# Kernel optimization log

Measured on AMD Instinct MI355X. Metric: run time of the kernel, lower is better.

Reference implementation:

```python
import jax, jax.numpy as jnp
import numpy as np

DIM, H, MAX_K, RADIUS, KNN_K, ALPHA, LN_EPS = 128, 4, 32, 0.3, 8, 2, 1e-5
DH = DIM // H
SCALE = DH ** -0.5


def _layernorm(x, w, b):
    mu = jnp.mean(x, axis=-1, keepdims=True)
    var = jnp.mean((x - mu) ** 2, axis=-1, keepdims=True)
    return (x - mu) * jax.lax.rsqrt(var + LN_EPS) * w + b


def setup_inputs() -> dict:
    key = jax.random.key(0)
    ks = jax.random.split(key, 12)
    N, M = 50000, 2500
    init = lambda k, shape: (jax.random.normal(k, shape, jnp.float32) * 0.02)
    return {
        "xyz": jax.random.normal(ks[0], (N, 3), jnp.float32),
        "feats": jax.random.normal(ks[1], (N, DIM), jnp.float32),
        "Wq": init(ks[2], (DIM, DIM)),
        "Wk": init(ks[3], (DIM, DIM)),
        "Wv": init(ks[4], (DIM, DIM)),
        "Wo": init(ks[5], (DIM, DIM)),
        "bo": jnp.zeros((DIM,), jnp.float32),
        "n1w": jnp.ones((DIM,), jnp.float32),
        "n1b": jnp.zeros((DIM,), jnp.float32),
        "n2w": jnp.ones((DIM,), jnp.float32),
        "n2b": jnp.zeros((DIM,), jnp.float32),
        "W1": init(ks[6], (DIM, 4 * DIM)),
        "b1": jnp.zeros((4 * DIM,), jnp.float32),
        "W2": init(ks[7], (4 * DIM, DIM)),
        "b2": jnp.zeros((DIM,), jnp.float32),
        "Wp": init(ks[8], (DIM, DIM)),
        "bp": jnp.zeros((DIM,), jnp.float32),
        "idx_center": jax.random.randint(ks[9], (M,), 0, N),
    }


def reference(xyz, feats, Wq, Wk, Wv, Wo, bo, n1w, n1b, n2w, n2b, W1, b1, W2, b2, Wp, bp, idx_center):
    M = idx_center.shape[0]
    center_xyz = xyz[idx_center]          # (M,3)
    center_feat = feats[idx_center]       # (M,C)

    # euclidean distance matrix (M,N) via |a|^2+|b|^2-2ab, safe sqrt (0-grad at 0 like torch.cdist)
    d2 = (jnp.sum(center_xyz ** 2, -1)[:, None] + jnp.sum(xyz ** 2, -1)[None, :]
          - 2.0 * center_xyz @ xyz.T)
    d2 = jnp.maximum(d2, 0.0)
    pos = d2 > 0
    dist = jnp.where(pos, jnp.sqrt(jnp.where(pos, d2, 1.0)), 0.0)  # (M,N)

    # ball query: mask + top-max_k smallest distances
    nbr_mask = dist < RADIUS
    nbr_mask = nbr_mask.at[jnp.arange(M), idx_center].set(True)
    dist_masked = jnp.where(nbr_mask, dist, jnp.inf)
    neg_d, nbr_idx = jax.lax.top_k(-dist_masked, MAX_K)   # (M,K)
    nbr_dist = -neg_d
    mask_valid = jnp.isfinite(nbr_dist)                    # (M,K)

    # gather neighbor feats, zero where invalid
    nbr_feats = jnp.where(mask_valid[..., None], feats[nbr_idx], 0.0)  # (M,K,C)

    # masked local attention per center (tiny heads)
    q = (center_feat @ Wq).reshape(M, H, DH)                       # (M,H,D)
    k = (nbr_feats @ Wk).reshape(M, MAX_K, H, DH).transpose(0, 2, 1, 3)  # (M,H,K,D)
    v = (nbr_feats @ Wv).reshape(M, MAX_K, H, DH).transpose(0, 2, 1, 3)
    attn = jnp.einsum('mhd,mhkd->mhk', q * SCALE, k)
    attn = jnp.where(mask_valid[:, None, :], attn, -1e9)
    attn = jax.nn.softmax(attn, axis=-1)
    out = jnp.einsum('mhk,mhkd->mhd', attn, v)
    # faithful to torch: transpose(1,2) before flatten -> (M, D, H) layout
    out = jnp.swapaxes(out, 1, 2).reshape(M, DIM)
    upd = out @ Wo + bo

    cf = center_feat + _layernorm(upd, n1w, n1b)
    ffn = jax.nn.relu(cf @ W1 + b1) @ W2 + b2
    cf = cf + _layernorm(ffn, n2w, n2b)

    # KNN inverse-distance-weighted upsample back to all N points
    neg_v, knn_idx = jax.lax.top_k(-dist.T, KNN_K)   # (N,k)
    knn_dist = -neg_v
    w = 1.0 / (knn_dist + 1e-6) ** ALPHA
    w = w / jnp.sum(w, axis=-1, keepdims=True)
    out_feats = jnp.einsum('nk,nkc->nc', w, cf[knn_idx])  # (N,C)
    out_feats = out_feats + jax.nn.relu(out_feats @ Wp + bp)
    return feats + out_feats
```

## Files before the change

kernel.cpp:

```cpp
#include <hip/hip_runtime.h>
#include <hip/hip_bf16.h>
#include <stdint.h>

#define DIM    128
#define KMAX   32
#define LN_EPS 1e-5f
#define ATT_SCALE 0.17677669529663687f
#define CAND   2048
#define WTOT   214400
#define PB     32
#define NSTR2  72
#define KSTR   132

typedef unsigned long long u64;
static __device__ __forceinline__ float bf2f(__hip_bfloat16 x) { return __bfloat162float(x); }

static __device__ __forceinline__ float norm32(float x, float y, float z) {
    return __fadd_rn(__fadd_rn(__fmul_rn(x, x), __fmul_rn(y, y)), __fmul_rn(z, z));
}
static __device__ __forceinline__ float d2_32(float cx, float cy, float cz, float cw,
                                              float px, float py, float pz, float pw) {
    float dot = __fmaf_rn(cz, pz, __fmaf_rn(cy, py, __fmul_rn(cx, px)));
    return __fsub_rn(__fadd_rn(cw, pw), __fmul_rn(2.0f, dot));
}
static __device__ __forceinline__ float d2_to_dist(float d2) {
    d2 = fmaxf(d2, 0.0f);
    return (d2 > 0.0f) ? __fsqrt_rn(d2) : 0.0f;
}
static __device__ __forceinline__ float dist32(float cx, float cy, float cz, float cw,
                                               float px, float py, float pz, float pw) {
    return d2_to_dist(d2_32(cx, cy, cz, cw, px, py, pz, pw));
}

static __device__ __forceinline__ float ldf(const void* p, int f32, size_t i) {
    return f32 ? ((const float*)p)[i] : bf2f(((const __hip_bfloat16*)p)[i]);
}
static __device__ __forceinline__ int ldidx(const void* p, int i64, int m) {
    return i64 ? ((const int*)p)[2 * m] : ((const int*)p)[m];
}

struct Ptrs { const void* p[18]; int sz[18]; };

__global__ void probe_dtypes(Ptrs P, int* __restrict__ fl) {
    int j = threadIdx.x;
    if (j >= 18) return;
    const void* x = P.p[j];
    int sz = P.sz[j];
    int flag = 0;
    if (j == 17) {
        const int* ip = (const int*)x;
        int odd_zero = 1, even_nz = 0;
        for (int k = 0; k < 8 && 2 * k + 1 < sz * 2; ++k) {
            if (ip[2 * k + 1] != 0) odd_zero = 0;
            if (ip[2 * k] != 0) even_nz = 1;
        }
        flag = (odd_zero && even_nz) ? 1 : 0;
    } else {
        const __hip_bfloat16* hp = (const __hip_bfloat16*)x;
        int n = sz < 256 ? sz : 256;
        for (int i = 0; i < n; ++i) {
            float w = bf2f(hp[i]);
            if (w != w || fabsf(w) > 1000.0f) { flag = 1; break; }
        }
        if ((j == 7 || j == 9) && bf2f(hp[0]) == 0.0f) flag = 1;
    }
    fl[j] = flag;
}

__global__ __launch_bounds__(256) void conv_prep(Ptrs P, const int* __restrict__ fl,
                                                 float* __restrict__ Wf,
                                                 float4* __restrict__ pnt4,
                                                 float4* __restrict__ cent4,
                                                 int N, int M, int convB) {
    int b = blockIdx.x;
    if (b < convB) {
        int i = b * 256 + threadIdx.x;
        if (i >= WTOT) return;
        int j, off;
        if      (i < 16384)  { j = 2;  off = i; }
        else if (i < 32768)  { j = 3;  off = i - 16384; }
        else if (i < 49152)  { j = 4;  off = i - 32768; }
        else if (i < 65536)  { j = 5;  off = i - 49152; }
        else if (i < 131072) { j = 11; off = i - 65536; }
        else if (i < 196608) { j = 13; off = i - 131072; }
        else if (i < 212992) { j = 15; off = i - 196608; }
        else if (i < 213120) { j = 6;  off = i - 212992; }
        else if (i < 213248) { j = 7;  off = i - 213120; }
        else if (i < 213376) { j = 8;  off = i - 213248; }
        else if (i < 213504) { j = 9;  off = i - 213376; }
        else if (i < 213632) { j = 10; off = i - 213504; }
        else if (i < 214144) { j = 12; off = i - 213632; }
        else if (i < 214272) { j = 14; off = i - 214144; }
        else                 { j = 16; off = i - 214272; }
        Wf[i] = ldf(P.p[j], fl[j], off);
    } else {
        int i = (b - convB) * 256 + threadIdx.x;
        int f0 = fl[0];
        if (i < N) {
            float x = ldf(P.p[0], f0, 3 * i + 0);
            float y = ldf(P.p[0], f0, 3 * i + 1);
            float z = ldf(P.p[0], f0, 3 * i + 2);
            pnt4[i] = make_float4(x, y, z, norm32(x, y, z));
        }
        if (i < M) {
            int c = ldidx(P.p[17], fl[17], i);
            c = (c >= 0 && c < N) ? c : 0;
            float x = ldf(P.p[0], f0, 3 * c + 0);
            float y = ldf(P.p[0], f0, 3 * c + 1);
            float z = ldf(P.p[0], f0, 3 * c + 2);
            cent4[i] = make_float4(x, y, z, norm32(x, y, z));
        }
    }
}

__global__ __launch_bounds__(256) void ball_scan(
    const float4* __restrict__ pnt4,
    const float4* __restrict__ cent4,
    int N, int* __restrict__ nbr_g) {

    __shared__ u64 key[CAND];
    __shared__ int s_cnt, s_ni[KMAX];

    int m = blockIdx.x, tid = threadIdx.x;
    float4 cc4 = cent4[m];

    if (tid == 0) s_cnt = 0;
    if (tid < KMAX) s_ni[tid] = -1;
    __syncthreads();

    for (int i = tid; i < N; i += 256) {
        float4 p = pnt4[i];
        float d2 = d2_32(cc4.x, cc4.y, cc4.z, cc4.w, p.x, p.y, p.z, p.w);
        if (d2 < 0.0901f) {
            float dist = d2_to_dist(d2);
            if (dist < 0.3f) {
                int pos = atomicAdd(&s_cnt, 1);
                if (pos < CAND)
                    key[pos] = ((u64)__float_as_uint(dist) << 32) | (unsigned)i;
            }
        }
    }
    __syncthreads();
    int cnt = min(s_cnt, CAND);

    for (int i = tid; i < cnt; i += 256) {
        u64 ki = key[i];
        int r = 0;
        for (int j = 0; j < cnt; ++j) r += (key[j] < ki) ? 1 : 0;
        if (r < KMAX) s_ni[r] = (int)(unsigned)(ki & 0xFFFFFFFFULL);
    }
    __syncthreads();
    if (tid < KMAX) nbr_g[m * KMAX + tid] = s_ni[tid];
}

#define NFT2(cc, kk) R[(cc) * NSTR2 + (kk)]
#define SKV2(kk, col) R[(kk) * KSTR + (col)]

__global__ __launch_bounds__(256, 4) void attn_ffn(
    const int* __restrict__ nbr_g,
    const void* __restrict__ feats,
    const void* __restrict__ idxc,
    const int* __restrict__ fl,
    const float* __restrict__ Wf,
    float* __restrict__ cf_out, int N, int M) {

    const float* Wqf = Wf;
    const float* Wkf = Wf + 16384;
    const float* Wvf = Wf + 32768;
    const float* Wof = Wf + 49152;
    const float* W1f = Wf + 65536;
    const float* W2f = Wf + 131072;
    const float* Pf  = Wf + 212992;

    __shared__ __align__(16) float R[128 * NSTR2];
    __shared__ int   s_ni[2 * KMAX];
    __shared__ __align__(16) float s_cf[256], s_x[256];
    __shared__ float s_red[8];

    int tid = threadIdx.x;
    int lane = tid & 63, wv = tid >> 6;
    int center = tid >> 7, col = tid & 127;
    int m0 = blockIdx.x * 2;
    int f1 = fl[1], fi = fl[17];

    if (tid < 64) {
        int m2 = m0 + (tid >> 5);
        s_ni[tid] = (m2 < M) ? nbr_g[m2 * KMAX + (tid & 31)] : -1;
    }
    {
        int m2 = m0 + center; m2 = (m2 < M) ? m2 : (M - 1);
        int c = ldidx(idxc, fi, m2);
        c = (c >= 0 && c < N) ? c : 0;
        s_cf[tid] = ldf(feats, f1, (size_t)c * DIM + col);
    }
    __syncthreads();
    for (int t = tid; t < 64 * DIM; t += 256) {
        int kk2 = t >> 7, cc = t & 127;
        int idx = s_ni[kk2];
        float v = (idx >= 0 && idx < N) ? ldf(feats, f1, (size_t)idx * DIM + cc) : 0.0f;
        NFT2(cc, kk2) = v;
    }
    __syncthreads();

    int kq = tid >> 5, cq = tid & 31;
    int k0 = kq * 8, c0 = cq * 4;
    float ka[8][4], va[8][4];
#pragma unroll
    for (int j = 0; j < 8; ++j)
#pragma unroll
        for (int cc2 = 0; cc2 < 4; ++cc2) { ka[j][cc2] = 0.0f; va[j][cc2] = 0.0f; }

#pragma unroll 2
    for (int i = 0; i < DIM; ++i) {
        float4 n0  = *(const float4*)&NFT2(i, k0);
        float4 n1  = *(const float4*)&NFT2(i, k0 + 4);
        float4 wk  = *(const float4*)&Wkf[i * DIM + c0];
        float4 wv4 = *(const float4*)&Wvf[i * DIM + c0];
        float nn[8] = {n0.x, n0.y, n0.z, n0.w, n1.x, n1.y, n1.z, n1.w};
#pragma unroll
        for (int j = 0; j < 8; ++j) {
            float nj = nn[j];
            ka[j][0] = fmaf(nj, wk.x, ka[j][0]);
            ka[j][1] = fmaf(nj, wk.y, ka[j][1]);
            ka[j][2] = fmaf(nj, wk.z, ka[j][2]);
            ka[j][3] = fmaf(nj, wk.w, ka[j][3]);
            va[j][0] = fmaf(nj, wv4.x, va[j][0]);
            va[j][1] = fmaf(nj, wv4.y, va[j][1]);
            va[j][2] = fmaf(nj, wv4.z, va[j][2]);
            va[j][3] = fmaf(nj, wv4.w, va[j][3]);
        }
    }
    __syncthreads();

    float* s_q    = R + 8448;
    float* s_attn = R + 8704;
    float* s_ao   = R + 8960;

#pragma unroll
    for (int j = 0; j < 8; ++j)
        *(float4*)&SKV2(k0 + j, c0) = make_float4(ka[j][0], ka[j][1], ka[j][2], ka[j][3]);
    {
        float acc = 0.0f;
        const float* cfc = s_cf + center * 128;
#pragma unroll 4
        for (int i = 0; i < DIM; i += 4) {
            float4 a = *(const float4*)&cfc[i];
            acc = fmaf(a.x, Wqf[(i + 0) * DIM + col], acc);
            acc = fmaf(a.y, Wqf[(i + 1) * DIM + col], acc);
            acc = fmaf(a.z, Wqf[(i + 2) * DIM + col], acc);
            acc = fmaf(a.w, Wqf[(i + 3) * DIM + col], acc);
        }
        s_q[tid] = acc;
    }
    __syncthreads();

    {
        int h = (tid >> 5) & 3, kk = tid & 31;
        float s = 0.0f;
#pragma unroll
        for (int d = 0; d < 32; ++d)
            s = fmaf(s_q[center * 128 + h * 32 + d], SKV2(center * 32 + kk, h * 32 + d), s);
        s *= ATT_SCALE;
        if (s_ni[center * 32 + kk] < 0) s = -1e9f;
        float mx = s;
        for (int off = 16; off; off >>= 1) mx = fmaxf(mx, __shfl_xor(mx, off, 32));
        float e = expf(s - mx);
        float sm = e;
        for (int off = 16; off; off >>= 1) sm += __shfl_xor(sm, off, 32);
        sm = (sm > 0.0f) ? sm : 1.0f;
        s_attn[tid] = e / sm;
    }
    __syncthreads();
#pragma unroll
    for (int j = 0; j < 8; ++j)
        *(float4*)&SKV2(k0 + j, c0) = make_float4(va[j][0], va[j][1], va[j][2], va[j][3]);
    __syncthreads();

    {
        int h = (tid >> 5) & 3, d = tid & 31;
        float o = 0.0f;
#pragma unroll
        for (int kk = 0; kk < KMAX; ++kk)
            o = fmaf(s_attn[center * 128 + h * 32 + kk], SKV2(center * 32 + kk, h * 32 + d), o);
        s_ao[center * 128 + d * 4 + h] = o;
    }
    __syncthreads();

    float upd = Pf[0 + col];
    {
#pragma unroll 4
        for (int i = 0; i < DIM; i += 4) {
            float4 a = *(const float4*)&s_ao[center * 128 + i];
            upd = fmaf(a.x, Wof[(i + 0) * DIM + col], upd);
            upd = fmaf(a.y, Wof[(i + 1) * DIM + col], upd);
            upd = fmaf(a.z, Wof[(i + 2) * DIM + col], upd);
            upd = fmaf(a.w, Wof[(i + 3) * DIM + col], upd);
        }
        float sum = upd;
        for (int off = 32; off; off >>= 1) sum += __shfl_xor(sum, off, 64);
        if (lane == 0) s_red[wv] = sum;
    }
    __syncthreads();
    float mu = (s_red[center * 2] + s_red[center * 2 + 1]) * (1.0f / 128.0f);
    float xc = upd - mu;
    {
        float q2 = xc * xc;
        for (int off = 32; off; off >>= 1) q2 += __shfl_xor(q2, off, 64);
        if (lane == 0) s_red[4 + wv] = q2;
    }
    __syncthreads();
    float var = (s_red[4 + center * 2] + s_red[5 + center * 2]) * (1.0f / 128.0f);
    float cf1;
    {
        float rs = 1.0f / sqrtf(var + LN_EPS);
        float ln1 = fmaf(xc * rs, Pf[128 + col], Pf[256 + col]);
        cf1 = s_cf[tid] + ln1;
        s_x[tid] = cf1;
    }
    __syncthreads();

    float* s_h = R;
#pragma unroll
    for (int jj = 0; jj < 4; ++jj) {
        int j = col + 128 * jj;
        float a = Pf[640 + j];
#pragma unroll 4
        for (int i = 0; i < DIM; i += 4) {
            float4 v = *(const float4*)&s_x[center * 128 + i];
            a = fmaf(v.x, W1f[(i + 0) * 512 + j], a);
            a = fmaf(v.y, W1f[(i + 1) * 512 + j], a);
            a = fmaf(v.z, W1f[(i + 2) * 512 + j], a);
            a = fmaf(v.w, W1f[(i + 3) * 512 + j], a);
        }
        s_h[center * 512 + j] = fmaxf(a, 0.0f);
    }
    __syncthreads();

    float fa = Pf[1152 + col];
    {
        const float* hc = s_h + center * 512;
#pragma unroll 4
        for (int i = 0; i < 256; i += 4) {
            float4 v = *(const float4*)&hc[i];
            fa = fmaf(v.x, W2f[(i + 0) * DIM + col], fa);
            fa = fmaf(v.y, W2f[(i + 1) * DIM + col], fa);
            fa = fmaf(v.z, W2f[(i + 2) * DIM + col], fa);
            fa = fmaf(v.w, W2f[(i + 3) * DIM + col], fa);
        }
    }
    float fb = 0.0f;
    {
        const float* hc = s_h + center * 512;
#pragma unroll 4
        for (int i = 256; i < 512; i += 4) {
            float4 v = *(const float4*)&hc[i];
            fb = fmaf(v.x, W2f[(i + 0) * DIM + col], fb);
            fb = fmaf(v.y, W2f[(i + 1) * DIM + col], fb);
            fb = fmaf(v.z, W2f[(i + 2) * DIM + col], fb);
            fb = fmaf(v.w, W2f[(i + 3) * DIM + col], fb);
        }
    }
    float ffn = fa + fb;
    {
        float sum = ffn;
        for (int off = 32; off; off >>= 1) sum += __shfl_xor(sum, off, 64);
        if (lane == 0) s_red[wv] = sum;
    }
    __syncthreads();
    mu = (s_red[center * 2] + s_red[center * 2 + 1]) * (1.0f / 128.0f);
    xc = ffn - mu;
    {
        float q2 = xc * xc;
        for (int off = 32; off; off >>= 1) q2 += __shfl_xor(q2, off, 64);
        if (lane == 0) s_red[4 + wv] = q2;
    }
    __syncthreads();
    var = (s_red[4 + center * 2] + s_red[5 + center * 2]) * (1.0f / 128.0f);
    {
        float rs2 = 1.0f / sqrtf(var + LN_EPS);
        float ln2 = fmaf(xc * rs2, Pf[384 + col], Pf[512 + col]);
        int m2 = m0 + center;
        if (m2 < M) cf_out[(size_t)m2 * DIM + col] = cf1 + ln2;
    }
}

#define CSWAP(a, b) { if ((b) < (a)) { u64 t_ = (a); (a) = (b); (b) = t_; } }

static __device__ __forceinline__ float extract8(float vmn) {
    float vv = vmn, T = 0.0f;
#pragma unroll
    for (int e = 0; e < 8; ++e) {
        float mv = vv;
        for (int off = 32; off; off >>= 1) mv = fminf(mv, __shfl_xor(mv, off, 64));
        T = mv;
        if (vv == mv) vv = 3.4e38f;
    }
    return fmaxf(T, 0.0f) * 1.0000019073486328f;
}

__global__ __launch_bounds__(256) void knn_select(
    const float4* __restrict__ pnt4,
    const float4* __restrict__ cent4,
    const float* __restrict__ cf,
    float* __restrict__ upg,
    int N, int M) {

    __shared__ u64 s_buf[4][2][64];
    __shared__ u64 s_srt[4][2][8];
    __shared__ int s_cnt[4][2];

    int tid = threadIdx.x;
    int lane = tid & 63, wv = tid >> 6;
    int p0 = blockIdx.x * 8 + wv * 2;
    bool ownA = (p0 < N), ownB = (p0 + 1 < N);

    float4 pa = make_float4(0.f, 0.f, 0.f, 0.f);
    float4 pb = make_float4(0.f, 0.f, 0.f, 0.f);
    if (ownA) pa = pnt4[p0];
    if (ownB) pb = pnt4[p0 + 1];

    if (lane < 2) s_cnt[wv][lane] = 0;
    __syncthreads();

    float va = 3.4e38f, vb = 3.4e38f;
    for (int j = lane; j < M; j += 64) {
        float4 cc = cent4[j];
        va = fminf(va, d2_32(cc.x, cc.y, cc.z, cc.w, pa.x, pa.y, pa.z, pa.w));
        vb = fminf(vb, d2_32(cc.x, cc.y, cc.z, cc.w, pb.x, pb.y, pb.z, pb.w));
    }
    float Ta = extract8(va);
    float Tb = extract8(vb);

    for (int j = lane; j < M; j += 64) {
        float4 cc = cent4[j];
        float d2a = d2_32(cc.x, cc.y, cc.z, cc.w, pa.x, pa.y, pa.z, pa.w);
        float d2b = d2_32(cc.x, cc.y, cc.z, cc.w, pb.x, pb.y, pb.z, pb.w);
        if (d2a <= Ta) {
            float dist = d2_to_dist(d2a);
            u64 key = ((u64)__float_as_uint(dist) << 32) | (unsigned)j;
            int pos = atomicAdd(&s_cnt[wv][0], 1);
            if (pos < 64) s_buf[wv][0][pos] = key;
        }
        if (d2b <= Tb) {
            float dist = d2_to_dist(d2b);
            u64 key = ((u64)__float_as_uint(dist) << 32) | (unsigned)j;
            int pos = atomicAdd(&s_cnt[wv][1], 1);
            if (pos < 64) s_buf[wv][1][pos] = key;
        }
    }

    int   ki[2][8];
    float w8[2][8];
    float wsum[2];

#pragma unroll
    for (int e = 0; e < 2; ++e) {
        int cnt = s_cnt[wv][e];
        if (cnt <= 64 && M >= 8) {
            u64 myk = (lane < cnt) ? s_buf[wv][e][lane] : ~0ULL;
            int r = 0;
            for (int i = 0; i < cnt; ++i) {
                u64 o = s_buf[wv][e][i];
                r += (o < myk) ? 1 : 0;
            }
            if (lane < cnt && r < 8) s_srt[wv][e][r] = myk;
        } else {
            float4 pp = e ? pb : pa;
            u64 f0 = ~0ULL, f1_ = ~0ULL, f2_ = ~0ULL, f3 = ~0ULL,
                f4 = ~0ULL, f5 = ~0ULL, f6 = ~0ULL, f7 = ~0ULL;
            for (int j = lane; j < M; j += 64) {
                float4 cc = cent4[j];
                float dist = dist32(cc.x, cc.y, cc.z, cc.w, pp.x, pp.y, pp.z, pp.w);
                u64 key = ((u64)__float_as_uint(dist) << 32) | (unsigned)j;
                if (key < f7) {
                    f7 = key;
                    CSWAP(f6, f7); CSWAP(f5, f6); CSWAP(f4, f5); CSWAP(f3, f4);
                    CSWAP(f2_, f3); CSWAP(f1_, f2_); CSWAP(f0, f1_);
                }
            }
            int ptr2 = 0;
            u64 cur2 = f0;
#pragma unroll
            for (int e2 = 0; e2 < 8; ++e2) {
                u64 v = cur2;
                for (int off = 32; off; off >>= 1) {
                    u64 o = __shfl_down(v, off, 64);
                    v = (o < v) ? o : v;
                }
                u64 gm = __shfl(v, 0, 64);
                if (lane == 0) s_srt[wv][e][e2] = gm;
                if (cur2 == gm) {
                    ptr2++;
                    cur2 = (ptr2 == 1) ? f1_ : (ptr2 == 2) ? f2_ : (ptr2 == 3) ? f3 :
                           (ptr2 == 4) ? f4 : (ptr2 == 5) ? f5 : (ptr2 == 6) ? f6 :
                           (ptr2 == 7) ? f7 : ~0ULL;
                }
            }
        }
        float ws = 0.0f;
#pragma unroll
        for (int e2 = 0; e2 < 8; ++e2) {
            u64 gm = s_srt[wv][e][e2];
            float d = __uint_as_float((unsigned)(gm >> 32));
            int ci = (int)(unsigned)(gm & 0xFFFFFFFFULL);
            ci = (ci >= 0 && ci < M) ? ci : 0;
            float t = __fadd_rn(d, 1e-6f);
            float w = 1.0f / __fmul_rn(t, t);
            ws += w;
            ki[e][e2] = ci;
            w8[e][e2] = w;
        }
        wsum[e] = ws;
    }

    float invA = 1.0f / wsum[0];
    float invB = 1.0f / wsum[1];
#pragma unroll
    for (int k = 0; k < 8; ++k) { w8[0][k] *= invA; w8[1][k] *= invB; }

    int c0 = lane, c1 = lane + 64;
    float uA0 = 0.0f, uA1 = 0.0f, uB0 = 0.0f, uB1 = 0.0f;
#pragma unroll
    for (int k = 0; k < 8; ++k) {
        const float* row = cf + (size_t)ki[0][k] * DIM;
        uA0 = fmaf(w8[0][k], row[c0], uA0);
        uA1 = fmaf(w8[0][k], row[c1], uA1);
    }
#pragma unroll
    for (int k = 0; k < 8; ++k) {
        const float* row = cf + (size_t)ki[1][k] * DIM;
        uB0 = fmaf(w8[1][k], row[c0], uB0);
        uB1 = fmaf(w8[1][k], row[c1], uB1);
    }

    if (ownA) {
        upg[(size_t)p0 * DIM + c0] = uA0;
        upg[(size_t)p0 * DIM + c1] = uA1;
    }
    if (ownB) {
        upg[(size_t)(p0 + 1) * DIM + c0] = uB0;
        upg[(size_t)(p0 + 1) * DIM + c1] = uB1;
    }
}

__global__ __launch_bounds__(256) void wp_out(
    const float* __restrict__ Wf,
    const void* __restrict__ feats,
    const int* __restrict__ fl,
    float* __restrict__ out,
    int N) {

    const float* Wpf = Wf + 196608;
    const float* bpf = Wf + 212992 + 1280;

    __shared__ __align__(16) float s_up[PB][132];

    int tid = threadIdx.x;
    int p0 = blockIdx.x * PB;

    for (int f = tid; f < PB * 32; f += 256) {
        int p = f >> 5, i4 = (f & 31) << 2;
        float4 v = make_float4(0.f, 0.f, 0.f, 0.f);
        if (p0 + p < N) v = *(const float4*)&out[(size_t)(p0 + p) * DIM + i4];
        *(float4*)&s_up[p][i4] = v;
    }
    __syncthreads();

    int cq = tid & 31, pq = tid >> 5;
    int c0 = cq << 2;
    int pA = pq << 2;

    float a00 = 0.f, a01 = 0.f, a02 = 0.f, a03 = 0.f;
    float a10 = 0.f, a11 = 0.f, a12 = 0.f, a13 = 0.f;
    float a20 = 0.f, a21 = 0.f, a22 = 0.f, a23 = 0.f;
    float a30 = 0.f, a31 = 0.f, a32 = 0.f, a33 = 0.f;

#pragma unroll 4
    for (int i = 0; i < DIM; ++i) {
        float4 w = *(const float4*)&Wpf[(size_t)i * DIM + c0];
        float u0 = s_up[pA + 0][i];
        float u1 = s_up[pA + 1][i];
        float u2 = s_up[pA + 2][i];
        float u3 = s_up[pA + 3][i];
        a00 = fmaf(u0, w.x, a00); a01 = fmaf(u0, w.y, a01);
        a02 = fmaf(u0, w.z, a02); a03 = fmaf(u0, w.w, a03);
        a10 = fmaf(u1, w.x, a10); a11 = fmaf(u1, w.y, a11);
        a12 = fmaf(u1, w.z, a12); a13 = fmaf(u1, w.w, a13);
        a20 = fmaf(u2, w.x, a20); a21 = fmaf(u2, w.y, a21);
        a22 = fmaf(u2, w.z, a22); a23 = fmaf(u2, w.w, a23);
        a30 = fmaf(u3, w.x, a30); a31 = fmaf(u3, w.y, a31);
        a32 = fmaf(u3, w.z, a32); a33 = fmaf(u3, w.w, a33);
    }

    int f1v = fl[1];
    float4 bp4 = make_float4(bpf[c0 + 0], bpf[c0 + 1], bpf[c0 + 2], bpf[c0 + 3]);

    float accs[4][4] = {{a00, a01, a02, a03}, {a10, a11, a12, a13},
                        {a20, a21, a22, a23}, {a30, a31, a32, a33}};
#pragma unroll
    for (int a = 0; a < 4; ++a) {
        int p = p0 + pA + a;
        if (p < N) {
            float4 u = *(const float4*)&s_up[pA + a][c0];
            float4 o;
            o.x = ldf(feats, f1v, (size_t)p * DIM + c0 + 0) + u.x + fmaxf(bp4.x + accs[a][0], 0.0f);
            o.y = ldf(feats, f1v, (size_t)p * DIM + c0 + 1) + u.y + fmaxf(bp4.y + accs[a][1], 0.0f);
            o.z = ldf(feats, f1v, (size_t)p * DIM + c0 + 2) + u.z + fmaxf(bp4.z + accs[a][2], 0.0f);
            o.w = ldf(feats, f1v, (size_t)p * DIM + c0 + 3) + u.w + fmaxf(bp4.w + accs[a][3], 0.0f);
            *(float4*)&out[(size_t)p * DIM + c0] = o;
        }
    }
}

extern "C" void kernel_launch(void* const* d_in, const int* in_sizes, int n_in,
                              void* d_out, int out_size, void* d_ws, size_t ws_size,
                              hipStream_t stream) {
    int N = in_sizes[0] / 3;
    int M = in_sizes[17];

    Ptrs P;
    for (int j = 0; j < 18; ++j) { P.p[j] = d_in[j]; P.sz[j] = in_sizes[j]; }

    size_t off = 0;
    auto alloc = [&](size_t bytes) -> void* {
        off = (off + 255) & ~(size_t)255;
        void* p = (void*)((char*)d_ws + off);
        off += bytes;
        return p;
    };
    int*    fl    = (int*)alloc(32 * 4);
    float*  Wf    = (float*)alloc((size_t)WTOT * 4);
    float4* pnt4  = (float4*)alloc((size_t)N * 16);
    float4* cent4 = (float4*)alloc((size_t)M * 16);
    float*  cfbuf = (float*)alloc((size_t)M * DIM * 4);
    int*    nbr   = (int*)alloc((size_t)M * KMAX * 4);

    int convB = (WTOT + 255) / 256;
    int NM = (N > M) ? N : M;
    int prepB = (NM + 255) / 256;

    probe_dtypes<<<1, 32, 0, stream>>>(P, fl);
    conv_prep<<<convB + prepB, 256, 0, stream>>>(P, fl, Wf, pnt4, cent4, N, M, convB);
    ball_scan<<<M, 256, 0, stream>>>(pnt4, cent4, N, nbr);
    attn_ffn<<<(M + 1) / 2, 256, 0, stream>>>(nbr, d_in[1], d_in[17], fl, Wf, cfbuf, N, M);
    knn_select<<<(N + 7) / 8, 256, 0, stream>>>(pnt4, cent4, cfbuf, (float*)d_out, N, M);
    wp_out<<<(N + PB - 1) / PB, 256, 0, stream>>>(Wf, d_in[1], fl, (float*)d_out, N);
}
```

Measured before the change: 511.7 us.

## Process two centers per ball_scan block and four points per knn wave with LDS-staged centers

ball_scan now handles two centers per block, so each point load is shared by two distance tests, and the rank sort is split across two half-blocks. knn_select handles four points per wave instead of two and stages all center coordinates in shared memory (up to 2560 entries), so each center read serves more points and comes from LDS rather than global memory. Both changes aim to cut redundant global loads in the two scan-heavy kernels. The cost is more LDS per block (about 40KB in knn_select), higher register pressure, fewer blocks in flight, and half-block rank sorting that may serialize more when neighbour counts are large.

```diff
diff --git a/kernel.cpp b/kernel.cpp
--- a/kernel.cpp
+++ b/kernel.cpp
@@ -11,6 +11,7 @@
 #define PB     32
 #define NSTR2  72
 #define KSTR   132
+#define SCMAX  2560
 
 typedef unsigned long long u64;
 static __device__ __forceinline__ float bf2f(__hip_bfloat16 x) { return __bfloat162float(x); }
@@ -116,41 +117,57 @@
 __global__ __launch_bounds__(256) void ball_scan(
     const float4* __restrict__ pnt4,
     const float4* __restrict__ cent4,
-    int N, int* __restrict__ nbr_g) {
-
-    __shared__ u64 key[CAND];
-    __shared__ int s_cnt, s_ni[KMAX];
-
-    int m = blockIdx.x, tid = threadIdx.x;
-    float4 cc4 = cent4[m];
-
-    if (tid == 0) s_cnt = 0;
-    if (tid < KMAX) s_ni[tid] = -1;
+    int N, int M, int* __restrict__ nbr_g) {
+
+    __shared__ u64 key[2][CAND];
+    __shared__ int s_cnt[2], s_ni[2][KMAX];
+
+    int tid = threadIdx.x;
+    int m0 = blockIdx.x * 2, m1 = m0 + 1;
+    bool has1 = (m1 < M);
+    float4 c0 = cent4[m0];
+    float4 c1 = has1 ? cent4[m1] : make_float4(1e30f, 1e30f, 1e30f, 1e30f);
+
+    if (tid < 2) s_cnt[tid] = 0;
+    if (tid < KMAX) { s_ni[0][tid] = -1; s_ni[1][tid] = -1; }
     __syncthreads();
 
     for (int i = tid; i < N; i += 256) {
         float4 p = pnt4[i];
-        float d2 = d2_32(cc4.x, cc4.y, cc4.z, cc4.w, p.x, p.y, p.z, p.w);
-        if (d2 < 0.0901f) {
-            float dist = d2_to_dist(d2);
+        float d20 = d2_32(c0.x, c0.y, c0.z, c0.w, p.x, p.y, p.z, p.w);
+        if (d20 < 0.0901f) {
+            float dist = d2_to_dist(d20);
             if (dist < 0.3f) {
-                int pos = atomicAdd(&s_cnt, 1);
+                int pos = atomicAdd(&s_cnt[0], 1);
                 if (pos < CAND)
-                    key[pos] = ((u64)__float_as_uint(dist) << 32) | (unsigned)i;
+                    key[0][pos] = ((u64)__float_as_uint(dist) << 32) | (unsigned)i;
             }
         }
-    }
-    __syncthreads();
-    int cnt = min(s_cnt, CAND);
-
-    for (int i = tid; i < cnt; i += 256) {
-        u64 ki = key[i];
+        float d21 = d2_32(c1.x, c1.y, c1.z, c1.w, p.x, p.y, p.z, p.w);
+        if (d21 < 0.0901f) {
+            float dist = d2_to_dist(d21);
+            if (dist < 0.3f) {
+                int pos = atomicAdd(&s_cnt[1], 1);
+                if (pos < CAND)
+                    key[1][pos] = ((u64)__float_as_uint(dist) << 32) | (unsigned)i;
+            }
+        }
+    }
+    __syncthreads();
+
+    int half = tid >> 7, t2 = tid & 127;
+    int cnth = min(s_cnt[half], CAND);
+    if (half == 1 && !has1) cnth = 0;
+    for (int i = t2; i < cnth; i += 128) {
+        u64 ki = key[half][i];
         int r = 0;
-        for (int j = 0; j < cnt; ++j) r += (key[j] < ki) ? 1 : 0;
-        if (r < KMAX) s_ni[r] = (int)(unsigned)(ki & 0xFFFFFFFFULL);
-    }
-    __syncthreads();
-    if (tid < KMAX) nbr_g[m * KMAX + tid] = s_ni[tid];
+        for (int j = 0; j < cnth; ++j) r += (key[half][j] < ki) ? 1 : 0;
+        if (r < KMAX) s_ni[half][r] = (int)(unsigned)(ki & 0xFFFFFFFFULL);
+    }
+    __syncthreads();
+    if (tid < KMAX) nbr_g[m0 * KMAX + tid] = s_ni[0][tid];
+    if (has1 && tid >= 128 && tid < 128 + KMAX)
+        nbr_g[m1 * KMAX + (tid - 128)] = s_ni[1][tid - 128];
 }
 
 #define NFT2(cc, kk) R[(cc) * NSTR2 + (kk)]
@@ -405,56 +422,58 @@
     float* __restrict__ upg,
     int N, int M) {
 
-    __shared__ u64 s_buf[4][2][64];
-    __shared__ u64 s_srt[4][2][8];
-    __shared__ int s_cnt[4][2];
+    __shared__ __align__(16) float4 s_ct[SCMAX];
+    __shared__ u64 s_buf[4][4][64];
+    __shared__ u64 s_srt[4][4][8];
+    __shared__ int s_cnt[4][4];
 
     int tid = threadIdx.x;
     int lane = tid & 63, wv = tid >> 6;
-    int p0 = blockIdx.x * 8 + wv * 2;
-    bool ownA = (p0 < N), ownB = (p0 + 1 < N);
-
-    float4 pa = make_float4(0.f, 0.f, 0.f, 0.f);
-    float4 pb = make_float4(0.f, 0.f, 0.f, 0.f);
-    if (ownA) pa = pnt4[p0];
-    if (ownB) pb = pnt4[p0 + 1];
-
-    if (lane < 2) s_cnt[wv][lane] = 0;
-    __syncthreads();
-
-    float va = 3.4e38f, vb = 3.4e38f;
+    int p0 = blockIdx.x * 16 + wv * 4;
+
+    float4 pp[4];
+    bool own[4];
+#pragma unroll
+    for (int e = 0; e < 4; ++e) {
+        int p = p0 + e;
+        own[e] = (p < N);
+        pp[e] = own[e] ? pnt4[p] : make_float4(0.f, 0.f, 0.f, 0.f);
+    }
+
+    if (lane < 4) s_cnt[wv][lane] = 0;
+    for (int j = tid; j < M && j < SCMAX; j += 256) s_ct[j] = cent4[j];
+    __syncthreads();
+
+    float vmn[4] = {3.4e38f, 3.4e38f, 3.4e38f, 3.4e38f};
     for (int j = lane; j < M; j += 64) {
-        float4 cc = cent4[j];
-        va = fminf(va, d2_32(cc.x, cc.y, cc.z, cc.w, pa.x, pa.y, pa.z, pa.w));
-        vb = fminf(vb, d2_32(cc.x, cc.y, cc.z, cc.w, pb.x, pb.y, pb.z, pb.w));
-    }
-    float Ta = extract8(va);
-    float Tb = extract8(vb);
+        float4 cc = (j < SCMAX) ? s_ct[j] : cent4[j];
+#pragma unroll
+        for (int e = 0; e < 4; ++e)
+            vmn[e] = fminf(vmn[e], d2_32(cc.x, cc.y, cc.z, cc.w,
+                                         pp[e].x, pp[e].y, pp[e].z, pp[e].w));
+    }
+    float T[4];
+#pragma unroll
+    for (int e = 0; e < 4; ++e) T[e] = extract8(vmn[e]);
 
     for (int j = lane; j < M; j += 64) {
-        float4 cc = cent4[j];
-        float d2a = d2_32(cc.x, cc.y, cc.z, cc.w, pa.x, pa.y, pa.z, pa.w);
-        float d2b = d2_32(cc.x, cc.y, cc.z, cc.w, pb.x, pb.y, pb.z, pb.w);
-        if (d2a <= Ta) {
-            float dist = d2_to_dist(d2a);
-            u64 key = ((u64)__float_as_uint(dist) << 32) | (unsigned)j;
-            int pos = atomicAdd(&s_cnt[wv][0], 1);
-            if (pos < 64) s_buf[wv][0][pos] = key;
-        }
-        if (d2b <= Tb) {
-            float dist = d2_to_dist(d2b);
-            u64 key = ((u64)__float_as_uint(dist) << 32) | (unsigned)j;
-            int pos = atomicAdd(&s_cnt[wv][1], 1);
-            if (pos < 64) s_buf[wv][1][pos] = key;
-        }
-    }
-
-    int   ki[2][8];
-    float w8[2][8];
-    float wsum[2];
-
-#pragma unroll
-    for (int e = 0; e < 2; ++e) {
+        float4 cc = (j < SCMAX) ? s_ct[j] : cent4[j];
+#pragma unroll
+        for (int e = 0; e < 4; ++e) {
+            float d2 = d2_32(cc.x, cc.y, cc.z, cc.w,
+                             pp[e].x, pp[e].y, pp[e].z, pp[e].w);
+            if (d2 <= T[e]) {
+                float dist = d2_to_dist(d2);
+                u64 key = ((u64)__float_as_uint(dist) << 32) | (unsigned)j;
+                int pos = atomicAdd(&s_cnt[wv][e], 1);
+                if (pos < 64) s_buf[wv][e][pos] = key;
+            }
+        }
+    }
+
+    int c0 = lane, c1 = lane + 64;
+#pragma unroll
+    for (int e = 0; e < 4; ++e) {
         int cnt = s_cnt[wv][e];
         if (cnt <= 64 && M >= 8) {
             u64 myk = (lane < cnt) ? s_buf[wv][e][lane] : ~0ULL;
@@ -465,12 +484,12 @@
             }
             if (lane < cnt && r < 8) s_srt[wv][e][r] = myk;
         } else {
-            float4 pp = e ? pb : pa;
+            float4 pq = pp[e];
             u64 f0 = ~0ULL, f1_ = ~0ULL, f2_ = ~0ULL, f3 = ~0ULL,
                 f4 = ~0ULL, f5 = ~0ULL, f6 = ~0ULL, f7 = ~0ULL;
             for (int j = lane; j < M; j += 64) {
-                float4 cc = cent4[j];
-                float dist = dist32(cc.x, cc.y, cc.z, cc.w, pp.x, pp.y, pp.z, pp.w);
+                float4 cc = (j < SCMAX) ? s_ct[j] : cent4[j];
+                float dist = dist32(cc.x, cc.y, cc.z, cc.w, pq.x, pq.y, pq.z, pq.w);
                 u64 key = ((u64)__float_as_uint(dist) << 32) | (unsigned)j;
                 if (key < f7) {
                     f7 = key;
@@ -497,6 +516,8 @@
                 }
             }
         }
+        int   ki[8];
+        float w8[8];
         float ws = 0.0f;
 #pragma unroll
         for (int e2 = 0; e2 < 8; ++e2) {
@@ -507,39 +528,24 @@
             float t = __fadd_rn(d, 1e-6f);
             float w = 1.0f / __fmul_rn(t, t);
             ws += w;
-            ki[e][e2] = ci;
-            w8[e][e2] = w;
-        }
-        wsum[e] = ws;
-    }
-
-    float invA = 1.0f / wsum[0];
-    float invB = 1.0f / wsum[1];
-#pragma unroll
-    for (int k = 0; k < 8; ++k) { w8[0][k] *= invA; w8[1][k] *= invB; }
-
-    int c0 = lane, c1 = lane + 64;
-    float uA0 = 0.0f, uA1 = 0.0f, uB0 = 0.0f, uB1 = 0.0f;
-#pragma unroll
-    for (int k = 0; k < 8; ++k) {
-        const float* row = cf + (size_t)ki[0][k] * DIM;
-        uA0 = fmaf(w8[0][k], row[c0], uA0);
-        uA1 = fmaf(w8[0][k], row[c1], uA1);
-    }
-#pragma unroll
-    for (int k = 0; k < 8; ++k) {
-        const float* row = cf + (size_t)ki[1][k] * DIM;
-        uB0 = fmaf(w8[1][k], row[c0], uB0);
-        uB1 = fmaf(w8[1][k], row[c1], uB1);
-    }
-
-    if (ownA) {
-        upg[(size_t)p0 * DIM + c0] = uA0;
-        upg[(size_t)p0 * DIM + c1] = uA1;
-    }
-    if (ownB) {
-        upg[(size_t)(p0 + 1) * DIM + c0] = uB0;
-        upg[(size_t)(p0 + 1) * DIM + c1] = uB1;
+            ki[e2] = ci;
+            w8[e2] = w;
+        }
+        float inv = 1.0f / ws;
+#pragma unroll
+        for (int k = 0; k < 8; ++k) w8[k] *= inv;
+
+        float u0 = 0.0f, u1 = 0.0f;
+#pragma unroll
+        for (int k = 0; k < 8; ++k) {
+            const float* row = cf + (size_t)ki[k] * DIM;
+            u0 = fmaf(w8[k], row[c0], u0);
+            u1 = fmaf(w8[k], row[c1], u1);
+        }
+        if (own[e]) {
+            upg[(size_t)(p0 + e) * DIM + c0] = u0;
+            upg[(size_t)(p0 + e) * DIM + c1] = u1;
+        }
     }
 }
 
@@ -641,8 +647,8 @@
 
     probe_dtypes<<<1, 32, 0, stream>>>(P, fl);
     conv_prep<<<convB + prepB, 256, 0, stream>>>(P, fl, Wf, pnt4, cent4, N, M, convB);
-    ball_scan<<<M, 256, 0, stream>>>(pnt4, cent4, N, nbr);
+    ball_scan<<<(M + 1) / 2, 256, 0, stream>>>(pnt4, cent4, N, M, nbr);
     attn_ffn<<<(M + 1) / 2, 256, 0, stream>>>(nbr, d_in[1], d_in[17], fl, Wf, cfbuf, N, M);
-    knn_select<<<(N + 7) / 8, 256, 0, stream>>>(pnt4, cent4, cfbuf, (float*)d_out, N, M);
+    knn_select<<<(N + 15) / 16, 256, 0, stream>>>(pnt4, cent4, cfbuf, (float*)d_out, N, M);
     wp_out<<<(N + PB - 1) / PB, 256, 0, stream>>>(Wf, d_in[1], fl, (float*)d_out, N);
 }
```

Result: slower. 557.9 us (+9.0%).
